# Performance work log

Measured on AMD Instinct MI355X. Metric: run time of the kernel, lower is better.

The kernel has to match this reference:

```python
import jax, jax.numpy as jnp
import numpy as np

B, T, H, V = 4, 512, 2048, 32000
BETA = 0.1
EPS = 1e-4


def setup_inputs() -> dict:
    key = jax.random.key(0)
    ks = jax.random.split(key, 8)
    scale = 0.02  # keep logits in a realistic range
    return {
        "_input": jax.random.normal(ks[0], (B * T, H), jnp.float32) * scale,
        "weight": jax.random.normal(ks[1], (V, H), jnp.float32) * scale,
        "attention_mask": jnp.ones((B, T), jnp.float32),
        "rewards": jax.random.normal(ks[2], (B,), jnp.float32),
        "bias": jax.random.normal(ks[3], (V,), jnp.float32) * scale,
        "ref_input": jax.random.normal(ks[4], (B * T, H), jnp.float32) * scale,
        "ref_weight": jax.random.normal(ks[5], (V, H), jnp.float32) * scale,
        "ref_bias": jax.random.normal(ks[6], (V,), jnp.float32) * scale,
    }


def reference(_input, weight, attention_mask, rewards, bias, ref_input, ref_weight, ref_bias):
    # Policy: fused linear + log-softmax over vocab
    logits = jnp.einsum("nh,vh->nv", _input, weight) + bias  # [B*T, V]
    log_probs = jax.nn.log_softmax(logits, axis=-1).reshape(B, T, V)

    chosen = jnp.argmax(log_probs, axis=-1)  # [B, T] int
    tok_lp = jnp.take_along_axis(log_probs, chosen[..., None], axis=-1)[..., 0]  # [B, T]

    # Reference model (no grad)
    ref_logits = jnp.einsum("nh,vh->nv", ref_input, ref_weight) + ref_bias
    ref_log_probs = jax.lax.stop_gradient(jax.nn.log_softmax(ref_logits, axis=-1)).reshape(B, T, V)
    ref_tok_lp = jnp.take_along_axis(ref_log_probs, chosen[..., None], axis=-1)[..., 0]

    # Group-normalized advantages (torch.std -> ddof=1)
    advantages = (rewards - rewards.mean()) / (jnp.std(rewards, ddof=1) + EPS)

    # ratio == 1 in fwd, grads flow through tok_lp
    ratio = jnp.exp(tok_lp - jax.lax.stop_gradient(tok_lp))
    policy_loss = -ratio * advantages[:, None]

    delta = ref_tok_lp - tok_lp
    kl_div = jnp.exp(delta) - delta - 1.0

    per_token_loss = policy_loss + BETA * kl_div
    masked_loss = per_token_loss * attention_mask
    seq_lengths = jnp.maximum(attention_mask.sum(), 1.0)
    loss = masked_loss.sum() / seq_lengths
    return loss
```

## Files before the change

### kernel.cpp

```cpp
#include <hip/hip_runtime.h>

#define Bb   4
#define Ts   512
#define Hh   2048
#define Vv   32000
#define Nn   2048
#define BETA 0.1f

#define CHUNKS 125
#define NPC    250

typedef _Float16 h8  __attribute__((ext_vector_type(8)));
typedef _Float16 h4v __attribute__((ext_vector_type(4)));
typedef float    f4  __attribute__((ext_vector_type(4)));

__device__ __forceinline__ int swz(int row, int k) {
    return row * 64 + (k ^ ((row & 7) << 3));
}

template<bool FAST>
__global__ __launch_bounds__(256, 2) void grpo_gemm(
    const float* __restrict__ inP, const float* __restrict__ wP, const float* __restrict__ bP,
    const float* __restrict__ inR, const float* __restrict__ wR, const float* __restrict__ bR,
    const _Float16* __restrict__ inP16, const _Float16* __restrict__ wP16,
    const _Float16* __restrict__ inR16, const _Float16* __restrict__ wR16,
    float* __restrict__ Pm, float* __restrict__ Ps, int* __restrict__ Pa,
    float* __restrict__ Rm, float* __restrict__ Rs, float* __restrict__ Ra)
{
    __shared__ __align__(16) unsigned short lds[24576];

    const int rowT  = blockIdx.x;
    const int chunk = blockIdx.y;
    const int tid   = threadIdx.x;
    const int lane  = tid & 63;
    const int wid   = tid >> 6;
    const int wr    = wid >> 1;
    const int wc    = wid & 1;
    const int lr    = lane & 15;
    const int lk    = lane >> 4;

    const int rowBase = rowT * 128;
    const int colBase = chunk * 256;

    f4 acc[2][4][4];

    auto mma_all = [&]() {
        #pragma unroll
        for (int ks = 0; ks < 2; ++ks) {
            h8 af[4];
            #pragma unroll
            for (int m = 0; m < 4; m++)
                af[m] = *reinterpret_cast<const h8*>(&lds[swz(wr * 64 + m * 16 + lr, ks * 32 + lk * 8)]);
            #pragma unroll
            for (int vt = 0; vt < 2; ++vt) {
                h8 wf[4];
                #pragma unroll
                for (int n = 0; n < 4; n++)
                    wf[n] = *reinterpret_cast<const h8*>(
                        &lds[8192 + vt * 8192 + swz(wc * 64 + n * 16 + lr, ks * 32 + lk * 8)]);
                #pragma unroll
                for (int m = 0; m < 4; m++)
                    #pragma unroll
                    for (int n = 0; n < 4; n++)
                        acc[vt][m][n] = __builtin_amdgcn_mfma_f32_16x16x32_f16(af[m], wf[n], acc[vt][m][n], 0, 0, 0);
            }
        }
    };

    auto pass_gemm = [&](const float* __restrict__ IN, const float* __restrict__ W,
                         const _Float16* __restrict__ IN16, const _Float16* __restrict__ W16) {
        #pragma unroll
        for (int vt = 0; vt < 2; ++vt)
            #pragma unroll
            for (int m = 0; m < 4; m++)
                #pragma unroll
                for (int n = 0; n < 4; n++) { f4 z = {0.f, 0.f, 0.f, 0.f}; acc[vt][m][n] = z; }

        if constexpr (FAST) {
            const int rsub = lane >> 3;
            const int ksrc = ((lane & 7) ^ rsub) << 3;
            const _Float16* aSrc[4]; const _Float16* w0Src[4]; const _Float16* w1Src[4];
            #pragma unroll
            for (int i = 0; i < 4; i++) {
                const int c = wid * 4 + i;
                const int r = c * 8 + rsub;
                aSrc[i]  = IN16 + (size_t)(rowBase + r) * Hh + ksrc;
                w0Src[i] = W16  + (size_t)(colBase + r) * Hh + ksrc;
                w1Src[i] = W16  + (size_t)(colBase + 128 + r) * Hh + ksrc;
            }
            for (int kt = 0; kt < Hh / 64; ++kt) {
                __syncthreads();
                #pragma unroll
                for (int i = 0; i < 4; i++) {
                    const int c = wid * 4 + i;
                    __builtin_amdgcn_global_load_lds(
                        (const __attribute__((address_space(1))) void*)(aSrc[i] + kt * 64),
                        (__attribute__((address_space(3))) void*)&lds[c * 512], 16, 0, 0);
                    __builtin_amdgcn_global_load_lds(
                        (const __attribute__((address_space(1))) void*)(w0Src[i] + kt * 64),
                        (__attribute__((address_space(3))) void*)&lds[8192 + c * 512], 16, 0, 0);
                    __builtin_amdgcn_global_load_lds(
                        (const __attribute__((address_space(1))) void*)(w1Src[i] + kt * 64),
                        (__attribute__((address_space(3))) void*)&lds[16384 + c * 512], 16, 0, 0);
                }
                __syncthreads();
                mma_all();
            }
        } else {
            const float* Ab = IN + (size_t)rowBase * Hh;
            const float* Wb = W  + (size_t)colBase * Hh;
            for (int kt = 0; kt < Hh / 64; ++kt) {
                __syncthreads();
                #pragma unroll
                for (int i = 0; i < 8; i++) {
                    int f = tid + i * 256;
                    int r = f >> 4, kk = (f & 15) << 2;
                    const float4 v = *reinterpret_cast<const float4*>(Ab + (size_t)r * Hh + kt * 64 + kk);
                    h4v h; h[0] = (_Float16)v.x; h[1] = (_Float16)v.y; h[2] = (_Float16)v.z; h[3] = (_Float16)v.w;
                    *reinterpret_cast<h4v*>(&lds[swz(r, kk)]) = h;
                }
                #pragma unroll
                for (int i = 0; i < 16; i++) {
                    int f = tid + i * 256;
                    int vt = f >> 11, g = f & 2047;
                    int r = g >> 4, kk = (g & 15) << 2;
                    const float4 v = *reinterpret_cast<const float4*>(Wb + (size_t)(vt * 128 + r) * Hh + kt * 64 + kk);
                    h4v h; h[0] = (_Float16)v.x; h[1] = (_Float16)v.y; h[2] = (_Float16)v.z; h[3] = (_Float16)v.w;
                    *reinterpret_cast<h4v*>(&lds[8192 + vt * 8192 + swz(r, kk)]) = h;
                }
                __syncthreads();
                mma_all();
            }
        }
    };

    float sM[16], sS[16]; int sA[16];
    #pragma unroll
    for (int s = 0; s < 16; s++) { sM[s] = -__builtin_inff(); sS[s] = 0.f; sA[s] = 0x7fffffff; }

    pass_gemm(inP, wP, inP16, wP16);
    #pragma unroll
    for (int vt = 0; vt < 2; ++vt) {
        float bn[4];
        #pragma unroll
        for (int n = 0; n < 4; n++) bn[n] = bP[colBase + vt * 128 + wc * 64 + n * 16 + lr];
        #pragma unroll
        for (int m = 0; m < 4; m++)
            #pragma unroll
            for (int n = 0; n < 4; n++) {
                const int vg = colBase + vt * 128 + wc * 64 + n * 16 + lr;
                #pragma unroll
                for (int r = 0; r < 4; r++) {
                    const int s = m * 4 + r;
                    const float v = acc[vt][m][n][r] + bn[n];
                    if (v > sM[s]) { sS[s] = sS[s] * __expf(sM[s] - v) + 1.f; sM[s] = v; sA[s] = vg; }
                    else           { sS[s] += __expf(v - sM[s]); }
                }
            }
    }

    int aWin[16];
    #pragma unroll
    for (int s = 0; s < 16; s++) {
        float M = sM[s], S = sS[s]; int A = sA[s];
        #pragma unroll
        for (int d = 1; d < 16; d <<= 1) {
            float oM = __shfl_xor(M, d), oS = __shfl_xor(S, d); int oA = __shfl_xor(A, d);
            if (oM > M || (oM == M && oA < A)) { S = S * __expf(M - oM) + oS; M = oM; A = oA; }
            else                               { S += oS * __expf(oM - M); }
        }
        aWin[s] = A;
        if (lr == 0) {
            const int row = rowBase + wr * 64 + (s >> 2) * 16 + lk * 4 + (s & 3);
            const size_t id = (size_t)(chunk * 2 + wc) * Nn + row;
            Pm[id] = M; Ps[id] = S; Pa[id] = A;
        }
    }

    float rM[16], rS[16], rT[16];
    #pragma unroll
    for (int s = 0; s < 16; s++) { rM[s] = -__builtin_inff(); rS[s] = 0.f; rT[s] = -1e30f; }

    pass_gemm(inR, wR, inR16, wR16);
    #pragma unroll
    for (int vt = 0; vt < 2; ++vt) {
        float bn[4];
        #pragma unroll
        for (int n = 0; n < 4; n++) bn[n] = bR[colBase + vt * 128 + wc * 64 + n * 16 + lr];
        #pragma unroll
        for (int m = 0; m < 4; m++)
            #pragma unroll
            for (int n = 0; n < 4; n++) {
                const int vg = colBase + vt * 128 + wc * 64 + n * 16 + lr;
                #pragma unroll
                for (int r = 0; r < 4; r++) {
                    const int s = m * 4 + r;
                    const float v = acc[vt][m][n][r] + bn[n];
                    if (v > rM[s]) { rS[s] = rS[s] * __expf(rM[s] - v) + 1.f; rM[s] = v; }
                    else           { rS[s] += __expf(v - rM[s]); }
                    if (vg == aWin[s]) rT[s] = v;
                }
            }
    }

    #pragma unroll
    for (int s = 0; s < 16; s++) {
        float M = rM[s], S = rS[s], Tv = rT[s];
        #pragma unroll
        for (int d = 1; d < 16; d <<= 1) {
            float oM = __shfl_xor(M, d), oS = __shfl_xor(S, d), oT = __shfl_xor(Tv, d);
            if (oM > M) { S = S * __expf(M - oM) + oS; M = oM; }
            else        { S += oS * __expf(oM - M); }
            Tv = fmaxf(Tv, oT);
        }
        if (lr == 0) {
            const int row = rowBase + wr * 64 + (s >> 2) * 16 + lk * 4 + (s & 3);
            const size_t id = (size_t)(chunk * 2 + wc) * Nn + row;
            Rm[id] = M; Rs[id] = S; Ra[id] = Tv;
        }
    }
}

__global__ __launch_bounds__(256) void cvt16(const float* __restrict__ s, _Float16* __restrict__ d, size_t n)
{
    size_t i = ((size_t)blockIdx.x * 256 + threadIdx.x) * 8;
    const size_t stride = (size_t)gridDim.x * 256 * 8;
    for (; i < n; i += stride) {
        const float4 a = *reinterpret_cast<const float4*>(s + i);
        const float4 b = *reinterpret_cast<const float4*>(s + i + 4);
        h8 h;
        h[0] = (_Float16)a.x; h[1] = (_Float16)a.y; h[2] = (_Float16)a.z; h[3] = (_Float16)a.w;
        h[4] = (_Float16)b.x; h[5] = (_Float16)b.y; h[6] = (_Float16)b.z; h[7] = (_Float16)b.w;
        *reinterpret_cast<h8*>(d + i) = h;
    }
}

__global__ __launch_bounds__(256) void grpo_combine(
    const float* __restrict__ Pm, const float* __restrict__ Ps, const int* __restrict__ Pa,
    const float* __restrict__ Rm, const float* __restrict__ Rs, const float* __restrict__ Ra,
    const float* __restrict__ amask, const float* __restrict__ rewards,
    float* __restrict__ accv)
{
    const int row = blockIdx.x * 256 + threadIdx.x;

    const float r0 = rewards[0], r1 = rewards[1], r2 = rewards[2], r3 = rewards[3];
    const float mean = 0.25f * (r0 + r1 + r2 + r3);
    const float var  = ((r0 - mean) * (r0 - mean) + (r1 - mean) * (r1 - mean) +
                        (r2 - mean) * (r2 - mean) + (r3 - mean) * (r3 - mean)) * (1.f / 3.f);
    const float inv  = 1.f / (sqrtf(var) + 1e-4f);
    const int   b    = row >> 9;
    const float advb = (b == 0 ? (r0 - mean) : b == 1 ? (r1 - mean) : b == 2 ? (r2 - mean) : (r3 - mean)) * inv;

    float M = -__builtin_inff(), S = 0.f; int A = 0x7fffffff, cwin = 0;
    for (int pc = 0; pc < NPC; ++pc) {
        const size_t id = (size_t)pc * Nn + row;
        const float m = Pm[id], s = Ps[id]; const int a = Pa[id];
        if (m > M || (m == M && a < A)) { S = S * expf(M - m) + s; M = m; A = a; cwin = pc; }
        else                            { S += s * expf(m - M); }
    }
    const float tok = -logf(S);

    float RM = -__builtin_inff(), RS = 0.f;
    for (int pc = 0; pc < NPC; ++pc) {
        const size_t id = (size_t)pc * Nn + row;
        const float m = Rm[id], s = Rs[id];
        if (m > RM) { RS = RS * expf(RM - m) + s; RM = m; }
        else        { RS += s * expf(m - RM); }
    }
    const float rtok = Ra[(size_t)cwin * Nn + row] - (RM + logf(RS));

    const float d  = rtok - tok;
    const float kl = expf(d) - d - 1.f;
    const float mk = amask[row];
    const float num = (-advb + BETA * kl) * mk;

    __shared__ float rN[256], rD[256];
    rN[threadIdx.x] = num; rD[threadIdx.x] = mk;
    __syncthreads();
    for (int o = 128; o > 0; o >>= 1) {
        if (threadIdx.x < o) { rN[threadIdx.x] += rN[threadIdx.x + o]; rD[threadIdx.x] += rD[threadIdx.x + o]; }
        __syncthreads();
    }
    if (threadIdx.x == 0) { atomicAdd(&accv[0], rN[0]); atomicAdd(&accv[1], rD[0]); }
}

__global__ void grpo_final(const float* __restrict__ accv, float* __restrict__ out) {
    out[0] = accv[0] / fmaxf(accv[1], 1.f);
}

extern "C" void kernel_launch(void* const* d_in, const int* in_sizes, int n_in,
                              void* d_out, int out_size, void* d_ws, size_t ws_size,
                              hipStream_t stream)
{
    (void)in_sizes; (void)n_in; (void)out_size;

    const float* inP = (const float*)d_in[0];
    const float* wP  = (const float*)d_in[1];
    const float* am  = (const float*)d_in[2];
    const float* rw  = (const float*)d_in[3];
    const float* bP  = (const float*)d_in[4];
    const float* inR = (const float*)d_in[5];
    const float* wR  = (const float*)d_in[6];
    const float* bR  = (const float*)d_in[7];
    float* out = (float*)d_out;

    char* w = (char*)d_ws;
    const size_t arr = (size_t)NPC * Nn * sizeof(float);
    float* Pm = (float*)w; w += arr;
    float* Ps = (float*)w; w += arr;
    int*   Pa = (int*)  w; w += arr;
    float* Rm = (float*)w; w += arr;
    float* Rs = (float*)w; w += arr;
    float* Ra = (float*)w; w += arr;
    float* accv = (float*)w; w += 256;

    const size_t fA = (size_t)Nn * Hh * sizeof(_Float16);
    const size_t fW = (size_t)Vv * Hh * sizeof(_Float16);
    const size_t need = (size_t)(w - (char*)d_ws) + 2 * fA + 2 * fW;
    const bool fast = (ws_size >= need);

    hipMemsetAsync(accv, 0, 2 * sizeof(float), stream);

    if (fast) {
        _Float16* inP16 = (_Float16*)w;            w += fA;
        _Float16* inR16 = (_Float16*)w;            w += fA;
        _Float16* wP16  = (_Float16*)w;            w += fW;
        _Float16* wR16  = (_Float16*)w;            w += fW;
        hipLaunchKernelGGL(cvt16, dim3(512),  dim3(256), 0, stream, inP, inP16, (size_t)Nn * Hh);
        hipLaunchKernelGGL(cvt16, dim3(512),  dim3(256), 0, stream, inR, inR16, (size_t)Nn * Hh);
        hipLaunchKernelGGL(cvt16, dim3(2048), dim3(256), 0, stream, wP,  wP16,  (size_t)Vv * Hh);
        hipLaunchKernelGGL(cvt16, dim3(2048), dim3(256), 0, stream, wR,  wR16,  (size_t)Vv * Hh);
        hipLaunchKernelGGL((grpo_gemm<true>), dim3(16, CHUNKS), dim3(256), 0, stream,
                           inP, wP, bP, inR, wR, bR, inP16, wP16, inR16, wR16,
                           Pm, Ps, Pa, Rm, Rs, Ra);
    } else {
        hipLaunchKernelGGL((grpo_gemm<false>), dim3(16, CHUNKS), dim3(256), 0, stream,
                           inP, wP, bP, inR, wR, bR,
                           (const _Float16*)nullptr, (const _Float16*)nullptr,
                           (const _Float16*)nullptr, (const _Float16*)nullptr,
                           Pm, Ps, Pa, Rm, Rs, Ra);
    }

    hipLaunchKernelGGL(grpo_combine, dim3(Nn / 256), dim3(256), 0, stream,
                       Pm, Ps, Pa, Rm, Rs, Ra, am, rw, accv);
    hipLaunchKernelGGL(grpo_final, dim3(1), dim3(1), 0, stream, accv, out);
}
```

Baseline: 1.432 ms.

## Double-buffer GEMM LDS staging, swizzle block order, fuse conversions, parallelize combine

The FAST GEMM path now stages K-tiles of 32 into two LDS buffers, so global-to-LDS loads of the next tile overlap MFMA work on the current one, and it raises wave priority around the MFMAs. Blocks use a 1D grid remapped so that neighbouring blocks spread across chunks, which is meant to improve L2 locality across XCDs. The four fp16 conversion launches become one launch. Partial results are stored row-major, and the combine kernel uses one wave per row with shuffle reductions in place of a serial loop, with the atomics and memset swapped for a final reduction kernel. The cost is more synchronisation points per K, because the tile is smaller, and extra launch complexity.

```diff
diff --git a/kernel.cpp b/kernel.cpp
--- a/kernel.cpp
+++ b/kernel.cpp
@@ -9,13 +9,14 @@
 
 #define CHUNKS 125
 #define NPC    250
+#define NT     64
 
 typedef _Float16 h8  __attribute__((ext_vector_type(8)));
 typedef _Float16 h4v __attribute__((ext_vector_type(4)));
 typedef float    f4  __attribute__((ext_vector_type(4)));
 
-__device__ __forceinline__ int swz(int row, int k) {
-    return row * 64 + (k ^ ((row & 7) << 3));
+__device__ __forceinline__ int swz32(int row, int k) {
+    return row * 32 + (k ^ (((row >> 1) & 3) << 3));
 }
 
 template<bool FAST>
@@ -29,8 +30,11 @@
 {
     __shared__ __align__(16) unsigned short lds[24576];
 
-    const int rowT  = blockIdx.x;
-    const int chunk = blockIdx.y;
+    const int bid   = blockIdx.x;
+    const int g     = (bid & 7) * 250 + (bid >> 3);
+    const int chunk = g >> 4;
+    const int rowT  = g & 15;
+
     const int tid   = threadIdx.x;
     const int lane  = tid & 63;
     const int wid   = tid >> 6;
@@ -44,27 +48,28 @@
 
     f4 acc[2][4][4];
 
-    auto mma_all = [&]() {
-        #pragma unroll
-        for (int ks = 0; ks < 2; ++ks) {
-            h8 af[4];
+    const int rdk = ((lr >> 1) & 3) << 3;
+
+    auto mma = [&](const int bufBase) {
+        h8 af[4];
+        #pragma unroll
+        for (int m = 0; m < 4; m++)
+            af[m] = *reinterpret_cast<const h8*>(&lds[bufBase + (wr * 64 + m * 16 + lr) * 32 + (lk * 8 ^ rdk)]);
+        __builtin_amdgcn_s_setprio(1);
+        #pragma unroll
+        for (int vt = 0; vt < 2; ++vt) {
+            h8 wf[4];
+            #pragma unroll
+            for (int n = 0; n < 4; n++)
+                wf[n] = *reinterpret_cast<const h8*>(
+                    &lds[bufBase + 4096 + (vt * 128 + wc * 64 + n * 16 + lr) * 32 + (lk * 8 ^ rdk)]);
             #pragma unroll
             for (int m = 0; m < 4; m++)
-                af[m] = *reinterpret_cast<const h8*>(&lds[swz(wr * 64 + m * 16 + lr, ks * 32 + lk * 8)]);
-            #pragma unroll
-            for (int vt = 0; vt < 2; ++vt) {
-                h8 wf[4];
                 #pragma unroll
                 for (int n = 0; n < 4; n++)
-                    wf[n] = *reinterpret_cast<const h8*>(
-                        &lds[8192 + vt * 8192 + swz(wc * 64 + n * 16 + lr, ks * 32 + lk * 8)]);
-                #pragma unroll
-                for (int m = 0; m < 4; m++)
-                    #pragma unroll
-                    for (int n = 0; n < 4; n++)
-                        acc[vt][m][n] = __builtin_amdgcn_mfma_f32_16x16x32_f16(af[m], wf[n], acc[vt][m][n], 0, 0, 0);
-            }
-        }
+                    acc[vt][m][n] = __builtin_amdgcn_mfma_f32_16x16x32_f16(af[m], wf[n], acc[vt][m][n], 0, 0, 0);
+        }
+        __builtin_amdgcn_s_setprio(0);
     };
 
     auto pass_gemm = [&](const float* __restrict__ IN, const float* __restrict__ W,
@@ -77,59 +82,51 @@
                 for (int n = 0; n < 4; n++) { f4 z = {0.f, 0.f, 0.f, 0.f}; acc[vt][m][n] = z; }
 
         if constexpr (FAST) {
-            const int rsub = lane >> 3;
-            const int ksrc = ((lane & 7) ^ rsub) << 3;
-            const _Float16* aSrc[4]; const _Float16* w0Src[4]; const _Float16* w1Src[4];
-            #pragma unroll
-            for (int i = 0; i < 4; i++) {
-                const int c = wid * 4 + i;
-                const int r = c * 8 + rsub;
-                aSrc[i]  = IN16 + (size_t)(rowBase + r) * Hh + ksrc;
-                w0Src[i] = W16  + (size_t)(colBase + r) * Hh + ksrc;
-                w1Src[i] = W16  + (size_t)(colBase + 128 + r) * Hh + ksrc;
-            }
-            for (int kt = 0; kt < Hh / 64; ++kt) {
+            const int rsub = lane >> 2;
+            const int ksrc = ((lane & 3) ^ ((lane >> 3) & 3)) << 3;
+            const _Float16* src[6]; int dOff[6];
+            #pragma unroll
+            for (int i = 0; i < 6; i++) {
+                const int c = wid * 6 + i;
+                dOff[i] = c * 512;
+                src[i] = (c < 8)
+                    ? IN16 + (size_t)(rowBase + c * 16 + rsub) * Hh + ksrc
+                    : W16  + (size_t)(colBase + (c - 8) * 16 + rsub) * Hh + ksrc;
+            }
+            auto stage = [&](const int bufBase, const int kt) {
+                #pragma unroll
+                for (int i = 0; i < 6; i++)
+                    __builtin_amdgcn_global_load_lds(
+                        (const __attribute__((address_space(1))) void*)(src[i] + kt * 32),
+                        (__attribute__((address_space(3))) void*)&lds[bufBase + dOff[i]], 16, 0, 0);
+            };
+            stage(0, 0);
+            __syncthreads();
+            for (int kt = 0; kt < NT; kt += 2) {
+                stage(12288, kt + 1);
+                mma(0);
                 __syncthreads();
-                #pragma unroll
-                for (int i = 0; i < 4; i++) {
-                    const int c = wid * 4 + i;
-                    __builtin_amdgcn_global_load_lds(
-                        (const __attribute__((address_space(1))) void*)(aSrc[i] + kt * 64),
-                        (__attribute__((address_space(3))) void*)&lds[c * 512], 16, 0, 0);
-                    __builtin_amdgcn_global_load_lds(
-                        (const __attribute__((address_space(1))) void*)(w0Src[i] + kt * 64),
-                        (__attribute__((address_space(3))) void*)&lds[8192 + c * 512], 16, 0, 0);
-                    __builtin_amdgcn_global_load_lds(
-                        (const __attribute__((address_space(1))) void*)(w1Src[i] + kt * 64),
-                        (__attribute__((address_space(3))) void*)&lds[16384 + c * 512], 16, 0, 0);
+                if (kt + 2 < NT) stage(0, kt + 2);
+                mma(12288);
+                __syncthreads();
+            }
+        } else {
+            for (int kt = 0; kt < NT; ++kt) {
+                __syncthreads();
+                #pragma unroll
+                for (int i = 0; i < 12; i++) {
+                    const int gq = tid + i * 256;
+                    int dst; const float* s;
+                    if (gq < 1024) { const int r = gq >> 3, kk = (gq & 7) << 2;
+                        s = IN + (size_t)(rowBase + r) * Hh + kt * 32 + kk; dst = swz32(r, kk); }
+                    else { const int gw = gq - 1024, r = gw >> 3, kk = (gw & 7) << 2;
+                        s = W + (size_t)(colBase + r) * Hh + kt * 32 + kk; dst = 4096 + swz32(r, kk); }
+                    const float4 v = *reinterpret_cast<const float4*>(s);
+                    h4v h; h[0] = (_Float16)v.x; h[1] = (_Float16)v.y; h[2] = (_Float16)v.z; h[3] = (_Float16)v.w;
+                    *reinterpret_cast<h4v*>(&lds[dst]) = h;
                 }
                 __syncthreads();
-                mma_all();
-            }
-        } else {
-            const float* Ab = IN + (size_t)rowBase * Hh;
-            const float* Wb = W  + (size_t)colBase * Hh;
-            for (int kt = 0; kt < Hh / 64; ++kt) {
-                __syncthreads();
-                #pragma unroll
-                for (int i = 0; i < 8; i++) {
-                    int f = tid + i * 256;
-                    int r = f >> 4, kk = (f & 15) << 2;
-                    const float4 v = *reinterpret_cast<const float4*>(Ab + (size_t)r * Hh + kt * 64 + kk);
-                    h4v h; h[0] = (_Float16)v.x; h[1] = (_Float16)v.y; h[2] = (_Float16)v.z; h[3] = (_Float16)v.w;
-                    *reinterpret_cast<h4v*>(&lds[swz(r, kk)]) = h;
-                }
-                #pragma unroll
-                for (int i = 0; i < 16; i++) {
-                    int f = tid + i * 256;
-                    int vt = f >> 11, g = f & 2047;
-                    int r = g >> 4, kk = (g & 15) << 2;
-                    const float4 v = *reinterpret_cast<const float4*>(Wb + (size_t)(vt * 128 + r) * Hh + kt * 64 + kk);
-                    h4v h; h[0] = (_Float16)v.x; h[1] = (_Float16)v.y; h[2] = (_Float16)v.z; h[3] = (_Float16)v.w;
-                    *reinterpret_cast<h4v*>(&lds[8192 + vt * 8192 + swz(r, kk)]) = h;
-                }
-                __syncthreads();
-                mma_all();
+                mma(0);
             }
         }
     };
@@ -172,7 +169,7 @@
         aWin[s] = A;
         if (lr == 0) {
             const int row = rowBase + wr * 64 + (s >> 2) * 16 + lk * 4 + (s & 3);
-            const size_t id = (size_t)(chunk * 2 + wc) * Nn + row;
+            const size_t id = (size_t)row * NPC + (chunk * 2 + wc);
             Pm[id] = M; Ps[id] = S; Pa[id] = A;
         }
     }
@@ -215,14 +212,25 @@
         }
         if (lr == 0) {
             const int row = rowBase + wr * 64 + (s >> 2) * 16 + lk * 4 + (s & 3);
-            const size_t id = (size_t)(chunk * 2 + wc) * Nn + row;
+            const size_t id = (size_t)row * NPC + (chunk * 2 + wc);
             Rm[id] = M; Rs[id] = S; Ra[id] = Tv;
         }
     }
 }
 
-__global__ __launch_bounds__(256) void cvt16(const float* __restrict__ s, _Float16* __restrict__ d, size_t n)
-{
+__global__ __launch_bounds__(256) void cvt_all(
+    const float* __restrict__ s0, _Float16* __restrict__ d0, size_t n0,
+    const float* __restrict__ s1, _Float16* __restrict__ d1, size_t n1,
+    const float* __restrict__ s2, _Float16* __restrict__ d2, size_t n2,
+    const float* __restrict__ s3, _Float16* __restrict__ d3, size_t n3)
+{
+    const float* s; _Float16* d; size_t n;
+    switch (blockIdx.y) {
+        case 0: s = s0; d = d0; n = n0; break;
+        case 1: s = s1; d = d1; n = n1; break;
+        case 2: s = s2; d = d2; n = n2; break;
+        default: s = s3; d = d3; n = n3; break;
+    }
     size_t i = ((size_t)blockIdx.x * 256 + threadIdx.x) * 8;
     const size_t stride = (size_t)gridDim.x * 256 * 8;
     for (; i < n; i += stride) {
@@ -235,57 +243,72 @@
     }
 }
 
-__global__ __launch_bounds__(256) void grpo_combine(
+__global__ __launch_bounds__(64) void grpo_combine(
     const float* __restrict__ Pm, const float* __restrict__ Ps, const int* __restrict__ Pa,
     const float* __restrict__ Rm, const float* __restrict__ Rs, const float* __restrict__ Ra,
     const float* __restrict__ amask, const float* __restrict__ rewards,
-    float* __restrict__ accv)
-{
-    const int row = blockIdx.x * 256 + threadIdx.x;
-
-    const float r0 = rewards[0], r1 = rewards[1], r2 = rewards[2], r3 = rewards[3];
-    const float mean = 0.25f * (r0 + r1 + r2 + r3);
-    const float var  = ((r0 - mean) * (r0 - mean) + (r1 - mean) * (r1 - mean) +
-                        (r2 - mean) * (r2 - mean) + (r3 - mean) * (r3 - mean)) * (1.f / 3.f);
-    const float inv  = 1.f / (sqrtf(var) + 1e-4f);
-    const int   b    = row >> 9;
-    const float advb = (b == 0 ? (r0 - mean) : b == 1 ? (r1 - mean) : b == 2 ? (r2 - mean) : (r3 - mean)) * inv;
-
-    float M = -__builtin_inff(), S = 0.f; int A = 0x7fffffff, cwin = 0;
-    for (int pc = 0; pc < NPC; ++pc) {
-        const size_t id = (size_t)pc * Nn + row;
-        const float m = Pm[id], s = Ps[id]; const int a = Pa[id];
-        if (m > M || (m == M && a < A)) { S = S * expf(M - m) + s; M = m; A = a; cwin = pc; }
-        else                            { S += s * expf(m - M); }
-    }
-    const float tok = -logf(S);
-
+    float* __restrict__ rowNum)
+{
+    const int row = blockIdx.x;
+    const int t   = threadIdx.x;
+    const size_t base = (size_t)row * NPC;
+
+    float M = -__builtin_inff(), S = 0.f; int A = 0x7fffffff; float Rv = -1e30f;
     float RM = -__builtin_inff(), RS = 0.f;
-    for (int pc = 0; pc < NPC; ++pc) {
-        const size_t id = (size_t)pc * Nn + row;
-        const float m = Rm[id], s = Rs[id];
-        if (m > RM) { RS = RS * expf(RM - m) + s; RM = m; }
-        else        { RS += s * expf(m - RM); }
-    }
-    const float rtok = Ra[(size_t)cwin * Nn + row] - (RM + logf(RS));
-
-    const float d  = rtok - tok;
-    const float kl = expf(d) - d - 1.f;
-    const float mk = amask[row];
-    const float num = (-advb + BETA * kl) * mk;
-
-    __shared__ float rN[256], rD[256];
-    rN[threadIdx.x] = num; rD[threadIdx.x] = mk;
+    #pragma unroll
+    for (int j = 0; j < 4; j++) {
+        const int pc = t + j * 64;
+        if (pc < NPC) {
+            const float m = Pm[base + pc], s = Ps[base + pc], rv = Ra[base + pc];
+            const int   a = Pa[base + pc];
+            if (m > M || (m == M && a < A)) { S = s + S * __expf(M - m); M = m; A = a; Rv = rv; }
+            else                            { S += s * __expf(m - M); }
+            const float rm = Rm[base + pc], rs = Rs[base + pc];
+            if (rm > RM) { RS = rs + RS * __expf(RM - rm); RM = rm; }
+            else         { RS += rs * __expf(rm - RM); }
+        }
+    }
+    #pragma unroll
+    for (int d = 1; d < 64; d <<= 1) {
+        const float oM = __shfl_xor(M, d), oS = __shfl_xor(S, d), oRv = __shfl_xor(Rv, d);
+        const int   oA = __shfl_xor(A, d);
+        if (oM > M || (oM == M && oA < A)) { S = oS + S * __expf(M - oM); M = oM; A = oA; Rv = oRv; }
+        else                               { S += oS * __expf(oM - M); }
+        const float orM = __shfl_xor(RM, d), orS = __shfl_xor(RS, d);
+        if (orM > RM) { RS = orS + RS * __expf(RM - orM); RM = orM; }
+        else          { RS += orS * __expf(orM - RM); }
+    }
+
+    if (t == 0) {
+        const float r0 = rewards[0], r1 = rewards[1], r2 = rewards[2], r3 = rewards[3];
+        const float mean = 0.25f * (r0 + r1 + r2 + r3);
+        const float var  = ((r0 - mean) * (r0 - mean) + (r1 - mean) * (r1 - mean) +
+                            (r2 - mean) * (r2 - mean) + (r3 - mean) * (r3 - mean)) * (1.f / 3.f);
+        const float inv  = 1.f / (sqrtf(var) + 1e-4f);
+        const int   b    = row >> 9;
+        const float advb = (b == 0 ? (r0 - mean) : b == 1 ? (r1 - mean) : b == 2 ? (r2 - mean) : (r3 - mean)) * inv;
+
+        const float tok  = -logf(S);
+        const float rtok = Rv - (RM + logf(RS));
+        const float dd   = rtok - tok;
+        const float kl   = expf(dd) - dd - 1.f;
+        rowNum[row] = (-advb + BETA * kl) * amask[row];
+    }
+}
+
+__global__ __launch_bounds__(256) void grpo_final(
+    const float* __restrict__ rowNum, const float* __restrict__ amask, float* __restrict__ out)
+{
+    __shared__ float sn[256], sd[256];
+    float n = 0.f, d = 0.f;
+    for (int i = threadIdx.x; i < Nn; i += 256) { n += rowNum[i]; d += amask[i]; }
+    sn[threadIdx.x] = n; sd[threadIdx.x] = d;
     __syncthreads();
     for (int o = 128; o > 0; o >>= 1) {
-        if (threadIdx.x < o) { rN[threadIdx.x] += rN[threadIdx.x + o]; rD[threadIdx.x] += rD[threadIdx.x + o]; }
+        if (threadIdx.x < o) { sn[threadIdx.x] += sn[threadIdx.x + o]; sd[threadIdx.x] += sd[threadIdx.x + o]; }
         __syncthreads();
     }
-    if (threadIdx.x == 0) { atomicAdd(&accv[0], rN[0]); atomicAdd(&accv[1], rD[0]); }
-}
-
-__global__ void grpo_final(const float* __restrict__ accv, float* __restrict__ out) {
-    out[0] = accv[0] / fmaxf(accv[1], 1.f);
+    if (threadIdx.x == 0) out[0] = sn[0] / fmaxf(sd[0], 1.f);
 }
 
 extern "C" void kernel_launch(void* const* d_in, const int* in_sizes, int n_in,
@@ -312,36 +335,35 @@
     float* Rm = (float*)w; w += arr;
     float* Rs = (float*)w; w += arr;
     float* Ra = (float*)w; w += arr;
-    float* accv = (float*)w; w += 256;
+    float* rowNum = (float*)w; w += ((size_t)Nn * sizeof(float) + 255) & ~(size_t)255;
 
     const size_t fA = (size_t)Nn * Hh * sizeof(_Float16);
     const size_t fW = (size_t)Vv * Hh * sizeof(_Float16);
     const size_t need = (size_t)(w - (char*)d_ws) + 2 * fA + 2 * fW;
     const bool fast = (ws_size >= need);
-
-    hipMemsetAsync(accv, 0, 2 * sizeof(float), stream);
 
     if (fast) {
         _Float16* inP16 = (_Float16*)w;            w += fA;
         _Float16* inR16 = (_Float16*)w;            w += fA;
         _Float16* wP16  = (_Float16*)w;            w += fW;
         _Float16* wR16  = (_Float16*)w;            w += fW;
-        hipLaunchKernelGGL(cvt16, dim3(512),  dim3(256), 0, stream, inP, inP16, (size_t)Nn * Hh);
-        hipLaunchKernelGGL(cvt16, dim3(512),  dim3(256), 0, stream, inR, inR16, (size_t)Nn * Hh);
-        hipLaunchKernelGGL(cvt16, dim3(2048), dim3(256), 0, stream, wP,  wP16,  (size_t)Vv * Hh);
-        hipLaunchKernelGGL(cvt16, dim3(2048), dim3(256), 0, stream, wR,  wR16,  (size_t)Vv * Hh);
-        hipLaunchKernelGGL((grpo_gemm<true>), dim3(16, CHUNKS), dim3(256), 0, stream,
+        hipLaunchKernelGGL(cvt_all, dim3(2048, 4), dim3(256), 0, stream,
+                           inP, inP16, (size_t)Nn * Hh,
+                           inR, inR16, (size_t)Nn * Hh,
+                           wP,  wP16,  (size_t)Vv * Hh,
+                           wR,  wR16,  (size_t)Vv * Hh);
+        hipLaunchKernelGGL((grpo_gemm<true>), dim3(16 * CHUNKS), dim3(256), 0, stream,
                            inP, wP, bP, inR, wR, bR, inP16, wP16, inR16, wR16,
                            Pm, Ps, Pa, Rm, Rs, Ra);
     } else {
-        hipLaunchKernelGGL((grpo_gemm<false>), dim3(16, CHUNKS), dim3(256), 0, stream,
+        hipLaunchKernelGGL((grpo_gemm<false>), dim3(16 * CHUNKS), dim3(256), 0, stream,
                            inP, wP, bP, inR, wR, bR,
                            (const _Float16*)nullptr, (const _Float16*)nullptr,
                            (const _Float16*)nullptr, (const _Float16*)nullptr,
                            Pm, Ps, Pa, Rm, Rs, Ra);
     }
 
-    hipLaunchKernelGGL(grpo_combine, dim3(Nn / 256), dim3(256), 0, stream,
-                       Pm, Ps, Pa, Rm, Rs, Ra, am, rw, accv);
-    hipLaunchKernelGGL(grpo_final, dim3(1), dim3(1), 0, stream, accv, out);
-}
+    hipLaunchKernelGGL(grpo_combine, dim3(Nn), dim3(64), 0, stream,
+                       Pm, Ps, Pa, Rm, Rs, Ra, am, rw, rowNum);
+    hipLaunchKernelGGL(grpo_final, dim3(1), dim3(256), 0, stream, rowNum, am, out);
+}
```

After: 1.414 ms. About the same (-1.3%).
